# Optimization experiments

Hardware: AMD Instinct MI355X
Metric: run time of the kernel (lower is better)

The kernel has to match this reference:

```python
import jax, jax.numpy as jnp
import numpy as np

NUM_HEADS = 8


def setup_inputs() -> dict:
    key = jax.random.key(0)
    ks = jax.random.split(key, 6)
    B, S, H = 2, 4096, 512
    Q = jax.random.normal(ks[0], (B, S, H), dtype=jnp.float32)
    K = jax.random.normal(ks[1], (B, S, H), dtype=jnp.float32)
    V = jax.random.normal(ks[2], (B, S, H), dtype=jnp.float32)
    risk_sigma = jax.random.uniform(ks[3], (B, 1), dtype=jnp.float32) * 0.2
    risk_lambda = jnp.array([2.0], dtype=jnp.float32)
    W_out = jax.random.normal(ks[4], (H, H), dtype=jnp.float32) * (1.0 / np.sqrt(H))
    b_out = jnp.zeros((H,), dtype=jnp.float32)
    return {"Q": Q, "K": K, "V": V, "risk_sigma": risk_sigma,
            "risk_lambda": risk_lambda, "W_out": W_out, "b_out": b_out}


def reference(Q, K, V, risk_sigma, risk_lambda, W_out, b_out):
    B, S, H = Q.shape
    nh = NUM_HEADS
    hd = H // nh
    # split heads: [B, S, nh, hd]
    q = Q.reshape(B, S, nh, hd)
    k = K.reshape(B, S, nh, hd)
    v = V.reshape(B, S, nh, hd)
    scale = 1.0 / jnp.sqrt(jnp.asarray(hd, dtype=Q.dtype))
    # [B, nh, S, S]
    scores = jnp.einsum('bshd,bthd->bhst', q, k) * scale
    # distance-based risk penalty
    pos = jnp.arange(S, dtype=Q.dtype)
    norm_dist = jnp.abs(pos[None, :] - pos[:, None]) / S  # [S, S]
    dist_sq = norm_dist ** 2
    sigma_c = jnp.clip(risk_sigma, 0.001, 0.2)            # [B, 1]
    sigma_n = (sigma_c - 0.001) / (0.2 - 0.001)
    lam = (risk_lambda / 10.0).reshape(())                 # scalar
    risk_term = lam * sigma_n[:, :, None, None] * dist_sq[None, None]  # [B,1,S,S]
    attn = jax.nn.softmax(scores - risk_term, axis=-1)
    ctx = jnp.einsum('bhst,bthd->bshd', attn, v).reshape(B, S, H)
    return ctx @ W_out.T + b_out
```

## Files before the change

kernel.cpp:

```cpp
#include <hip/hip_runtime.h>
#include <hip/hip_bf16.h>


#define S_LEN 4096
#define NHEAD 8
#define HD 64
#define HTOT 512

typedef __attribute__((ext_vector_type(8))) short short8;
typedef __attribute__((ext_vector_type(4))) float floatx4;
typedef __attribute__((ext_vector_type(8))) _Float16 half8;
typedef __attribute__((ext_vector_type(2))) _Float16 half2v;

#if __has_builtin(__builtin_amdgcn_exp2f)
#define EXP2F(x) __builtin_amdgcn_exp2f(x)
#else
#define EXP2F(x) exp2f(x)
#endif

__device__ __forceinline__ unsigned pack_bf16(float a, float b) {
    unsigned ua = __builtin_bit_cast(unsigned, a) + 0x8000u;
    unsigned ub = __builtin_bit_cast(unsigned, b) + 0x8000u;
    return __builtin_amdgcn_perm(ub, ua, 0x07060302u);
}

__device__ __forceinline__ unsigned short f2bf(float x) {
    unsigned u = __builtin_bit_cast(unsigned, x) + 0x8000u;
    return (unsigned short)(u >> 16);
}

__device__ __forceinline__ void async16(const unsigned short* g, unsigned short* l) {
    __builtin_amdgcn_global_load_lds(
        (const __attribute__((address_space(1))) unsigned int*)g,
        (__attribute__((address_space(3))) unsigned int*)l, 16, 0, 0);
}

__global__ __launch_bounds__(256) void prep_kernel(
    const float* __restrict__ K, unsigned short* __restrict__ K16,
    const float* __restrict__ V, unsigned short* __restrict__ Vt,
    const float* __restrict__ W, unsigned short* __restrict__ W16)
{
    const int tid = threadIdx.x;
    if (blockIdx.x >= 3072) {
        size_t i = ((size_t)(blockIdx.x - 3072) * 256 + tid) * 8;
        float4 a = *(const float4*)(W + i);
        float4 b = *(const float4*)(W + i + 4);
        unsigned o[4] = {pack_bf16(a.x, a.y), pack_bf16(a.z, a.w),
                         pack_bf16(b.x, b.y), pack_bf16(b.z, b.w)};
        *(short8*)(W16 + i) = *(short8*)o;
    } else if (blockIdx.x < 2048) {
        size_t i = ((size_t)blockIdx.x * 256 + tid) * 8;
        float4 a = *(const float4*)(K + i);
        float4 b = *(const float4*)(K + i + 4);
        unsigned o[4] = {pack_bf16(a.x, a.y), pack_bf16(a.z, a.w),
                         pack_bf16(b.x, b.y), pack_bf16(b.z, b.w)};
        *(short8*)(K16 + i) = *(short8*)o;
    } else {
        __shared__ unsigned short T[64 * 66];
        const int blk = blockIdx.x - 2048;
        const int st = blk & 63;
        const int bh = blk >> 6;
        const int b = bh >> 3, h = bh & 7;
        const float* src = V + ((size_t)b * S_LEN + st * 64) * HTOT + h * HD;
        for (int i = 0; i < 4; i++) {
            int idx = tid + i * 256;
            int s = idx >> 4, c4 = idx & 15;
            float4 v = *(const float4*)(src + (size_t)s * HTOT + c4 * 4);
            T[(c4 * 4 + 0) * 66 + s] = f2bf(v.x);
            T[(c4 * 4 + 1) * 66 + s] = f2bf(v.y);
            T[(c4 * 4 + 2) * 66 + s] = f2bf(v.z);
            T[(c4 * 4 + 3) * 66 + s] = f2bf(v.w);
        }
        __syncthreads();
        unsigned short* dst = Vt + ((size_t)bh * 64) * S_LEN + st * 64;
        for (int i = 0; i < 2; i++) {
            int idx = tid + i * 256;
            int d = idx >> 3, c8 = idx & 7;
            uint2 lo = *(const uint2*)&T[d * 66 + c8 * 8];
            uint2 hi = *(const uint2*)&T[d * 66 + c8 * 8 + 4];
            unsigned o[4] = {lo.x, lo.y, hi.x, hi.y};
            *(short8*)(dst + (size_t)d * S_LEN + c8 * 8) = *(short8*)o;
        }
    }
}

__global__ __launch_bounds__(256) void attn_kernel(
    const float* __restrict__ Q, const unsigned short* __restrict__ K16,
    const unsigned short* __restrict__ Vt,
    const float* __restrict__ risk_sigma, const float* __restrict__ risk_lambda,
    _Float16* __restrict__ Cpart, float* __restrict__ Lpart)
{
    __shared__ unsigned short QPsh[128 * 72];
    __shared__ unsigned short Ksh[2][64 * 64];
    __shared__ unsigned short Vsh[2][64 * 64];

    const int tid  = threadIdx.x;
    const int wave = tid >> 6;
    const int lane = tid & 63;
    const int quad = lane >> 4;
    const int ln   = lane & 15;
    const int sw   = ln & 7;

    const int bid = blockIdx.x;
    const int ks  = bid & 1;
    const int qt  = (bid >> 1) & 31;
    const int h   = (bid >> 6) & 7;
    const int b   = bid >> 9;
    const int qbase = qt * 128;

    float sig = risk_sigma[b];
    sig = fminf(fmaxf(sig, 0.001f), 0.2f);
    const float sn   = (sig - 0.001f) * (1.0f / 0.199f);
    const float coef = risk_lambda[0] * 0.1f * sn;
    const float nc2 = -coef * (1.0f / 4096.0f) * (1.0f / 4096.0f) * 1.4426950408889634f;
    const float qscale = 0.125f * 1.4426950408889634f;

    const float* Qb = Q + (size_t)b * S_LEN * HTOT + (size_t)h * HD;
    const unsigned short* Kb = K16 + (size_t)b * S_LEN * HTOT + (size_t)h * HD;
    const unsigned short* Vb = Vt + ((size_t)(b * 8 + h) * 64) * S_LEN;

    const int rl  = lane >> 3;
    const int c8g = ((lane & 7) ^ rl) << 3;
    auto dma = [&](int buf, int kbase) {
        const unsigned short* gk = Kb + (size_t)(kbase + wave * 8 + rl) * HTOT + c8g;
        const unsigned short* gv = Vb + (size_t)(wave * 8 + rl) * S_LEN + kbase + c8g;
        async16(gk,              &Ksh[buf][wave * 512 + lane * 8]);
        async16(gk + 32 * HTOT,  &Ksh[buf][(wave + 4) * 512 + lane * 8]);
        async16(gv,              &Vsh[buf][wave * 512 + lane * 8]);
        async16(gv + 32 * S_LEN, &Vsh[buf][(wave + 4) * 512 + lane * 8]);
    };

    dma(0, ks * 2048);
    for (int i = 0; i < 8; i++) {
        int idx = tid + i * 256;
        int r = idx >> 4, c4 = idx & 15;
        float4 v = *(const float4*)(Qb + (size_t)(qbase + r) * HTOT + c4 * 4);
        uint2 o;
        o.x = pack_bf16(v.x * qscale, v.y * qscale);
        o.y = pack_bf16(v.z * qscale, v.w * qscale);
        *(uint2*)&QPsh[r * 72 + c4 * 4] = o;
    }
    __syncthreads();

    short8 qf[2][2];
    for (int nt = 0; nt < 2; nt++) {
        qf[nt][0] = *(const short8*)&QPsh[(wave * 32 + nt * 16 + ln) * 72 + quad * 8];
        qf[nt][1] = *(const short8*)&QPsh[(wave * 32 + nt * 16 + ln) * 72 + 32 + quad * 8];
    }
    unsigned short* Pw = &QPsh[wave * 32 * 72];

    const short sone = (short)0x3F80;
    const short8 ones = {sone, sone, sone, sone, sone, sone, sone, sone};

    floatx4 Oacc[2][4], Lacc[2];
    for (int nt = 0; nt < 2; nt++) {
        Lacc[nt] = (floatx4){0.f, 0.f, 0.f, 0.f};
        for (int dt = 0; dt < 4; dt++) Oacc[nt][dt] = (floatx4){0.f, 0.f, 0.f, 0.f};
    }

    const int qa = qbase + wave * 32;

    for (int kt = 0; kt < 32; ++kt) {
        const int kbase = ks * 2048 + kt * 64;
        const int cur = kt & 1;
        if (kt < 31) dma(1 - cur, kbase + 64);
        const unsigned short* Kc = Ksh[cur];
        const unsigned short* Vc = Vsh[cur];

        const float dq = (float)(qa + ln - kbase);
        for (int jt = 0; jt < 4; jt++) {
            const int krow = (jt * 16 + ln) * 64;
            short8 ak0 = *(const short8*)&Kc[krow + ((quad ^ sw) << 3)];
            short8 ak1 = *(const short8*)&Kc[krow + (((quad + 4) ^ sw) << 3)];
            #pragma unroll
            for (int nt = 0; nt < 2; nt++) {
                floatx4 s = (floatx4){0.f, 0.f, 0.f, 0.f};
                s = __builtin_amdgcn_mfma_f32_16x16x32_bf16(ak0, qf[nt][0], s, 0, 0, 0);
                s = __builtin_amdgcn_mfma_f32_16x16x32_bf16(ak1, qf[nt][1], s, 0, 0, 0);
                float d = dq + (float)(nt * 16 - jt * 16 - quad * 4);
                float p[4];
                #pragma unroll
                for (int r = 0; r < 4; r++) {
                    float arg = __builtin_fmaf(nc2, d * d, s[r]);
                    p[r] = EXP2F(arg);
                    d -= 1.0f;
                }
                uint2 o;
                o.x = pack_bf16(p[0], p[1]);
                o.y = pack_bf16(p[2], p[3]);
                *(uint2*)&Pw[(nt * 16 + ln) * 72 + jt * 16 + quad * 4] = o;
            }
        }
        asm volatile("s_waitcnt lgkmcnt(0)" ::: "memory");
        __builtin_amdgcn_wave_barrier();

        short8 pf[2][2];
        for (int nt = 0; nt < 2; nt++) {
            pf[nt][0] = *(const short8*)&Pw[(nt * 16 + ln) * 72 + quad * 8];
            pf[nt][1] = *(const short8*)&Pw[(nt * 16 + ln) * 72 + 32 + quad * 8];
        }
        for (int dt = 0; dt < 4; dt++) {
            const int vrow = (dt * 16 + ln) * 64;
            short8 bv0 = *(const short8*)&Vc[vrow + ((quad ^ sw) << 3)];
            short8 bv1 = *(const short8*)&Vc[vrow + (((quad + 4) ^ sw) << 3)];
            #pragma unroll
            for (int nt = 0; nt < 2; nt++) {
                Oacc[nt][dt] = __builtin_amdgcn_mfma_f32_16x16x32_bf16(pf[nt][0], bv0, Oacc[nt][dt], 0, 0, 0);
                Oacc[nt][dt] = __builtin_amdgcn_mfma_f32_16x16x32_bf16(pf[nt][1], bv1, Oacc[nt][dt], 0, 0, 0);
            }
        }
        #pragma unroll
        for (int nt = 0; nt < 2; nt++) {
            Lacc[nt] = __builtin_amdgcn_mfma_f32_16x16x32_bf16(pf[nt][0], ones, Lacc[nt], 0, 0, 0);
            Lacc[nt] = __builtin_amdgcn_mfma_f32_16x16x32_bf16(pf[nt][1], ones, Lacc[nt], 0, 0, 0);
        }
        __syncthreads();
    }

    _Float16* Cw = Cpart + (size_t)bid * (128 * 64);
    for (int nt = 0; nt < 2; nt++) {
        if (ln == 0) {
            #pragma unroll
            for (int r = 0; r < 4; r++)
                Lpart[bid * 128 + wave * 32 + nt * 16 + quad * 4 + r] = Lacc[nt][r];
        }
        float rl4[4];
        #pragma unroll
        for (int r = 0; r < 4; r++) rl4[r] = 1.0f / Lacc[nt][r];
        for (int dt = 0; dt < 4; dt++)
            #pragma unroll
            for (int r = 0; r < 4; r++) {
                int q = wave * 32 + nt * 16 + quad * 4 + r;
                Cw[q * 64 + dt * 16 + ln] = (_Float16)(Oacc[nt][dt][r] * rl4[r]);
            }
    }
}

__global__ __launch_bounds__(256) void combine_kernel(
    const _Float16* __restrict__ Cpart, const float* __restrict__ Lpart,
    unsigned short* __restrict__ ctx)
{
    const int t = threadIdx.x;
    const int tile = blockIdx.x;
    const int qt = tile & 31, h = (tile >> 5) & 7, b = tile >> 8;
    __shared__ float w0s[128], w1s[128];
    if (t < 128) {
        float l0 = Lpart[(tile * 2 + 0) * 128 + t];
        float l1 = Lpart[(tile * 2 + 1) * 128 + t];
        float inv = 1.0f / (l0 + l1);
        w0s[t] = l0 * inv;
        w1s[t] = l1 * inv;
    }
    __syncthreads();
    const _Float16* C0 = Cpart + (size_t)(tile * 2) * (128 * 64);
    const _Float16* C1 = C0 + 128 * 64;
    for (int i = 0; i < 8; i++) {
        int e = (i * 256 + t) * 4;
        int q = e >> 6, d = e & 63;
        half2v a0 = *(const half2v*)(C0 + e);
        half2v a1 = *(const half2v*)(C0 + e + 2);
        half2v b0 = *(const half2v*)(C1 + e);
        half2v b1 = *(const half2v*)(C1 + e + 2);
        float w0 = w0s[q], w1 = w1s[q];
        float v0 = w0 * (float)a0[0] + w1 * (float)b0[0];
        float v1 = w0 * (float)a0[1] + w1 * (float)b0[1];
        float v2 = w0 * (float)a1[0] + w1 * (float)b1[0];
        float v3 = w0 * (float)a1[1] + w1 * (float)b1[1];
        uint2 o;
        o.x = pack_bf16(v0, v1);
        o.y = pack_bf16(v2, v3);
        *(uint2*)&ctx[((size_t)b * S_LEN + qt * 128 + q) * HTOT + h * HD + d] = o;
    }
}

__global__ __launch_bounds__(256) void proj_kernel(
    const unsigned short* __restrict__ A,
    const unsigned short* __restrict__ W16,
    const float* __restrict__ bias,
    float* __restrict__ out)
{
    __shared__ unsigned short Ash[2][64 * 32];
    __shared__ unsigned short Bsh[2][128 * 32];
    const int tid = threadIdx.x;
    const int wave = tid >> 6, lane = tid & 63, quad = lane >> 4, ln = lane & 15;
    const int wr = wave >> 1, wc = wave & 1;
    const int m0 = blockIdx.y * 64;
    const int nb = blockIdx.x * 128;

    const int arow = (wave * 64 + lane) >> 2;
    const int ac   = (wave * 64 + lane) & 3;
    const int acs  = (ac ^ ((arow >> 1) & 3)) << 3;
    const int wrow0 = (wave * 64 + lane) >> 2;
    const int wc0   = (wave * 64 + lane) & 3;
    const int wcs0  = (wc0 ^ ((wrow0 >> 1) & 3)) << 3;
    const int wrow1 = wrow0 + 64;
    const int wcs1  = (wc0 ^ ((wrow1 >> 1) & 3)) << 3;

    auto dma = [&](int buf, int k0) {
        async16(A + (size_t)(m0 + arow) * 512 + k0 + acs,
                &Ash[buf][wave * 512 + lane * 8]);
        async16(W16 + (size_t)(nb + wrow0) * 512 + k0 + wcs0,
                &Bsh[buf][wave * 512 + lane * 8]);
        async16(W16 + (size_t)(nb + wrow1) * 512 + k0 + wcs1,
                &Bsh[buf][(wave + 4) * 512 + lane * 8]);
    };

    floatx4 acc[2][4];
    for (int i = 0; i < 2; i++)
        for (int j = 0; j < 4; j++) acc[i][j] = (floatx4){0.f, 0.f, 0.f, 0.f};

    dma(0, 0);
    for (int kt = 0; kt < 16; ++kt) {
        const int cur = kt & 1;
        __syncthreads();
        if (kt < 15) dma(1 - cur, (kt + 1) * 32);

        short8 af[2], bf[4];
        for (int i = 0; i < 2; i++) {
            int r = wr * 32 + i * 16 + ln;
            af[i] = *(const short8*)&Ash[cur][r * 32 + ((quad ^ ((r >> 1) & 3)) << 3)];
        }
        for (int j = 0; j < 4; j++) {
            int r = wc * 64 + j * 16 + ln;
            bf[j] = *(const short8*)&Bsh[cur][r * 32 + ((quad ^ ((r >> 1) & 3)) << 3)];
        }
        for (int i = 0; i < 2; i++)
            for (int j = 0; j < 4; j++)
                acc[i][j] = __builtin_amdgcn_mfma_f32_16x16x32_bf16(af[i], bf[j], acc[i][j], 0, 0, 0);
    }

    for (int i = 0; i < 2; i++) {
        int row = m0 + wr * 32 + i * 16 + quad * 4;
        for (int j = 0; j < 4; j++) {
            int col = nb + wc * 64 + j * 16 + ln;
            float bv = bias[col];
            #pragma unroll
            for (int r = 0; r < 4; r++)
                out[(size_t)(row + r) * 512 + col] = acc[i][j][r] + bv;
        }
    }
}

extern "C" void kernel_launch(void* const* d_in, const int* in_sizes, int n_in,
                              void* d_out, int out_size, void* d_ws, size_t ws_size,
                              hipStream_t stream) {
    const float* Q    = (const float*)d_in[0];
    const float* K    = (const float*)d_in[1];
    const float* V    = (const float*)d_in[2];
    const float* sig  = (const float*)d_in[3];
    const float* lam  = (const float*)d_in[4];
    const float* W    = (const float*)d_in[5];
    const float* bias = (const float*)d_in[6];

    unsigned short* K16 = (unsigned short*)d_ws;
    unsigned short* Vt  = (unsigned short*)((char*)d_ws + (8u << 20));
    unsigned short* ctx = (unsigned short*)((char*)d_ws + (16u << 20));
    float* Lpart        = (float*)((char*)d_ws + (24u << 20));
    unsigned short* W16 = (unsigned short*)((char*)d_ws + (24u << 20) + (512u << 10));
    _Float16* Cpart     = (_Float16*)d_out;
    float* out = (float*)d_out;

    prep_kernel<<<dim3(3200), dim3(256), 0, stream>>>(K, K16, V, Vt, W, W16);
    attn_kernel<<<dim3(1024), dim3(256), 0, stream>>>(Q, K16, Vt, sig, lam, Cpart, Lpart);
    combine_kernel<<<dim3(512), dim3(256), 0, stream>>>(Cpart, Lpart, ctx);
    proj_kernel<<<dim3(4, 128), dim3(256), 0, stream>>>(ctx, W16, bias, out);
}
```

Baseline: 228.7 us.

## Keep P tile in registers by permuting K rows, drop LDS round-trip

K rows are loaded into shared memory in a permuted order, so the S=K·Q MFMA output lanes line up with the A-operand layout of the P·V MFMA. P then stays in registers instead of being written to and re-read from LDS. Q fragments are loaded straight from global memory into registers, which removes the QP shared buffer. The risk term is also folded into the MFMA accumulator initialiser, and the change adds setprio around the PV MFMAs and launch_bounds(256,4). The risk is register pressure under the 4-blocks occupancy hint, and the row-permutation mapping has to be exactly right to stay correct.

```diff
diff --git a/kernel.cpp b/kernel.cpp
--- a/kernel.cpp
+++ b/kernel.cpp
@@ -9,7 +9,6 @@
 
 typedef __attribute__((ext_vector_type(8))) short short8;
 typedef __attribute__((ext_vector_type(4))) float floatx4;
-typedef __attribute__((ext_vector_type(8))) _Float16 half8;
 typedef __attribute__((ext_vector_type(2))) _Float16 half2v;
 
 #if __has_builtin(__builtin_amdgcn_exp2f)
@@ -84,13 +83,12 @@
     }
 }
 
-__global__ __launch_bounds__(256) void attn_kernel(
+__global__ __launch_bounds__(256, 4) void attn_kernel(
     const float* __restrict__ Q, const unsigned short* __restrict__ K16,
     const unsigned short* __restrict__ Vt,
     const float* __restrict__ risk_sigma, const float* __restrict__ risk_lambda,
     _Float16* __restrict__ Cpart, float* __restrict__ Lpart)
 {
-    __shared__ unsigned short QPsh[128 * 72];
     __shared__ unsigned short Ksh[2][64 * 64];
     __shared__ unsigned short Vsh[2][64 * 64];
 
@@ -121,44 +119,54 @@
 
     const int rl  = lane >> 3;
     const int c8g = ((lane & 7) ^ rl) << 3;
-    auto dma = [&](int buf, int kbase) {
-        const unsigned short* gk = Kb + (size_t)(kbase + wave * 8 + rl) * HTOT + c8g;
-        const unsigned short* gv = Vb + (size_t)(wave * 8 + rl) * S_LEN + kbase + c8g;
-        async16(gk,              &Ksh[buf][wave * 512 + lane * 8]);
-        async16(gk + 32 * HTOT,  &Ksh[buf][(wave + 4) * 512 + lane * 8]);
+    const int ksrow = ((wave & 1) << 4) | (((rl >> 2) & 1) << 3)
+                    | ((wave >> 1) << 2) | (rl & 3);
+
+    auto dma = [&](int buf, int kb) {
+        const unsigned short* gv = Vb + (size_t)(wave * 8 + rl) * S_LEN + kb + c8g;
+        async16(Kb + (size_t)(kb + ksrow) * HTOT + c8g,
+                &Ksh[buf][wave * 512 + lane * 8]);
+        async16(Kb + (size_t)(kb + 32 + ksrow) * HTOT + c8g,
+                &Ksh[buf][(wave + 4) * 512 + lane * 8]);
         async16(gv,              &Vsh[buf][wave * 512 + lane * 8]);
         async16(gv + 32 * S_LEN, &Vsh[buf][(wave + 4) * 512 + lane * 8]);
     };
 
     dma(0, ks * 2048);
-    for (int i = 0; i < 8; i++) {
-        int idx = tid + i * 256;
-        int r = idx >> 4, c4 = idx & 15;
-        float4 v = *(const float4*)(Qb + (size_t)(qbase + r) * HTOT + c4 * 4);
-        uint2 o;
-        o.x = pack_bf16(v.x * qscale, v.y * qscale);
-        o.y = pack_bf16(v.z * qscale, v.w * qscale);
-        *(uint2*)&QPsh[r * 72 + c4 * 4] = o;
+
+    short8 qf[2][2];
+    {
+        const float* qp0 = Qb + (size_t)(qbase + wave * 32 + ln) * HTOT + quad * 8;
+        #pragma unroll
+        for (int nt = 0; nt < 2; nt++) {
+            const float* qp = qp0 + (size_t)(nt * 16) * HTOT;
+            #pragma unroll
+            for (int half = 0; half < 2; half++) {
+                float4 x = *(const float4*)(qp + half * 32);
+                float4 y = *(const float4*)(qp + half * 32 + 4);
+                unsigned o[4] = {pack_bf16(x.x * qscale, x.y * qscale),
+                                 pack_bf16(x.z * qscale, x.w * qscale),
+                                 pack_bf16(y.x * qscale, y.y * qscale),
+                                 pack_bf16(y.z * qscale, y.w * qscale)};
+                qf[nt][half] = *(short8*)o;
+            }
+        }
     }
     __syncthreads();
-
-    short8 qf[2][2];
-    for (int nt = 0; nt < 2; nt++) {
-        qf[nt][0] = *(const short8*)&QPsh[(wave * 32 + nt * 16 + ln) * 72 + quad * 8];
-        qf[nt][1] = *(const short8*)&QPsh[(wave * 32 + nt * 16 + ln) * 72 + 32 + quad * 8];
-    }
-    unsigned short* Pw = &QPsh[wave * 32 * 72];
 
     const short sone = (short)0x3F80;
     const short8 ones = {sone, sone, sone, sone, sone, sone, sone, sone};
 
     floatx4 Oacc[2][4], Lacc[2];
+    #pragma unroll
     for (int nt = 0; nt < 2; nt++) {
         Lacc[nt] = (floatx4){0.f, 0.f, 0.f, 0.f};
+        #pragma unroll
         for (int dt = 0; dt < 4; dt++) Oacc[nt][dt] = (floatx4){0.f, 0.f, 0.f, 0.f};
     }
 
     const int qa = qbase + wave * 32;
+    const float quad8f = (float)(quad * 8);
 
     for (int kt = 0; kt < 32; ++kt) {
         const int kbase = ks * 2048 + kt * 64;
@@ -167,53 +175,57 @@
         const unsigned short* Kc = Ksh[cur];
         const unsigned short* Vc = Vsh[cur];
 
-        const float dq = (float)(qa + ln - kbase);
+        const float dqq = (float)(qa + ln - kbase) - quad8f;
+        unsigned pw[2][2][4];
+
+        #pragma unroll
         for (int jt = 0; jt < 4; jt++) {
             const int krow = (jt * 16 + ln) * 64;
             short8 ak0 = *(const short8*)&Kc[krow + ((quad ^ sw) << 3)];
             short8 ak1 = *(const short8*)&Kc[krow + (((quad + 4) ^ sw) << 3)];
+            const float jtoff = (float)((jt >> 1) * 32 + (jt & 1) * 4);
             #pragma unroll
             for (int nt = 0; nt < 2; nt++) {
-                floatx4 s = (floatx4){0.f, 0.f, 0.f, 0.f};
-                s = __builtin_amdgcn_mfma_f32_16x16x32_bf16(ak0, qf[nt][0], s, 0, 0, 0);
-                s = __builtin_amdgcn_mfma_f32_16x16x32_bf16(ak1, qf[nt][1], s, 0, 0, 0);
-                float d = dq + (float)(nt * 16 - jt * 16 - quad * 4);
-                float p[4];
+                float d = dqq + ((float)(nt * 16) - jtoff);
+                floatx4 rk;
                 #pragma unroll
                 for (int r = 0; r < 4; r++) {
-                    float arg = __builtin_fmaf(nc2, d * d, s[r]);
-                    p[r] = EXP2F(arg);
+                    rk[r] = (nc2 * d) * d;
                     d -= 1.0f;
                 }
-                uint2 o;
-                o.x = pack_bf16(p[0], p[1]);
-                o.y = pack_bf16(p[2], p[3]);
-                *(uint2*)&Pw[(nt * 16 + ln) * 72 + jt * 16 + quad * 4] = o;
+                floatx4 s = __builtin_amdgcn_mfma_f32_16x16x32_bf16(ak0, qf[nt][0], rk, 0, 0, 0);
+                s = __builtin_amdgcn_mfma_f32_16x16x32_bf16(ak1, qf[nt][1], s, 0, 0, 0);
+                float p0 = EXP2F(s[0]);
+                float p1 = EXP2F(s[1]);
+                float p2 = EXP2F(s[2]);
+                float p3 = EXP2F(s[3]);
+                pw[nt][jt >> 1][(jt & 1) * 2 + 0] = pack_bf16(p0, p1);
+                pw[nt][jt >> 1][(jt & 1) * 2 + 1] = pack_bf16(p2, p3);
             }
         }
-        asm volatile("s_waitcnt lgkmcnt(0)" ::: "memory");
-        __builtin_amdgcn_wave_barrier();
-
-        short8 pf[2][2];
-        for (int nt = 0; nt < 2; nt++) {
-            pf[nt][0] = *(const short8*)&Pw[(nt * 16 + ln) * 72 + quad * 8];
-            pf[nt][1] = *(const short8*)&Pw[(nt * 16 + ln) * 72 + 32 + quad * 8];
-        }
+
+        __builtin_amdgcn_s_setprio(1);
+        #pragma unroll
         for (int dt = 0; dt < 4; dt++) {
             const int vrow = (dt * 16 + ln) * 64;
             short8 bv0 = *(const short8*)&Vc[vrow + ((quad ^ sw) << 3)];
             short8 bv1 = *(const short8*)&Vc[vrow + (((quad + 4) ^ sw) << 3)];
             #pragma unroll
             for (int nt = 0; nt < 2; nt++) {
-                Oacc[nt][dt] = __builtin_amdgcn_mfma_f32_16x16x32_bf16(pf[nt][0], bv0, Oacc[nt][dt], 0, 0, 0);
-                Oacc[nt][dt] = __builtin_amdgcn_mfma_f32_16x16x32_bf16(pf[nt][1], bv1, Oacc[nt][dt], 0, 0, 0);
+                short8 pa0 = *(const short8*)&pw[nt][0][0];
+                short8 pa1 = *(const short8*)&pw[nt][1][0];
+                Oacc[nt][dt] = __builtin_amdgcn_mfma_f32_16x16x32_bf16(pa0, bv0, Oacc[nt][dt], 0, 0, 0);
+                Oacc[nt][dt] = __builtin_amdgcn_mfma_f32_16x16x32_bf16(pa1, bv1, Oacc[nt][dt], 0, 0, 0);
             }
         }
         #pragma unroll
         for (int nt = 0; nt < 2; nt++) {
-            Lacc[nt] = __builtin_amdgcn_mfma_f32_16x16x32_bf16(pf[nt][0], ones, Lacc[nt], 0, 0, 0);
-            Lacc[nt] = __builtin_amdgcn_mfma_f32_16x16x32_bf16(pf[nt][1], ones, Lacc[nt], 0, 0, 0);
-        }
+            short8 pa0 = *(const short8*)&pw[nt][0][0];
+            short8 pa1 = *(const short8*)&pw[nt][1][0];
+            Lacc[nt] = __builtin_amdgcn_mfma_f32_16x16x32_bf16(pa0, ones, Lacc[nt], 0, 0, 0);
+            Lacc[nt] = __builtin_amdgcn_mfma_f32_16x16x32_bf16(pa1, ones, Lacc[nt], 0, 0, 0);
+        }
+        __builtin_amdgcn_s_setprio(0);
         __syncthreads();
     }
 
```

Result: faster. 205.8 us (-10.0%).
